# Kernel optimization log

Measured on AMD Instinct MI355X. Metric: run time of the kernel, lower is better.

The kernel has to match this reference:

```python
import jax, jax.numpy as jnp
import numpy as np

D = 2048
H = 32
EPS = 1e-5


def _ln(z, scale, bias):
    m = jnp.mean(z, axis=-1, keepdims=True)
    v = jnp.mean(jnp.square(z - m), axis=-1, keepdims=True)
    return (z - m) / jnp.sqrt(v + EPS) * scale + bias


def setup_inputs() -> dict:
    key = jax.random.key(0)
    ks = jax.random.split(key, 12)
    B, S = 4, 1024
    s = 0.02
    return {
        "x": jax.random.normal(ks[0], (B, S, D), jnp.float32),
        "Wq": jax.random.normal(ks[1], (D, D), jnp.float32) * s,
        "Wk": jax.random.normal(ks[2], (D, D), jnp.float32) * s,
        "Wv": jax.random.normal(ks[3], (D, D), jnp.float32) * s,
        "ln1_scale": jnp.ones((D,), jnp.float32) + jax.random.normal(ks[4], (D,), jnp.float32) * s,
        "ln1_bias": jax.random.normal(ks[5], (D,), jnp.float32) * s,
        "ln2_scale": jnp.ones((D,), jnp.float32) + jax.random.normal(ks[6], (D,), jnp.float32) * s,
        "ln2_bias": jax.random.normal(ks[7], (D,), jnp.float32) * s,
        "ff1_w": jax.random.normal(ks[8], (D, D), jnp.float32) * s,
        "ff1_b": jax.random.normal(ks[9], (D,), jnp.float32) * s,
        "ff2_w": jax.random.normal(ks[10], (D, D), jnp.float32) * s,
        "ff2_b": jax.random.normal(ks[11], (D,), jnp.float32) * s,
    }


def reference(x, Wq, Wk, Wv, ln1_scale, ln1_bias, ln2_scale, ln2_bias,
              ff1_w, ff1_b, ff2_w, ff2_b):
    B, S, _ = x.shape
    hd = D // H
    residual = x
    h = _ln(x, ln1_scale, ln1_bias)
    # QKV projections (no bias, per source)
    q = (h @ Wq).reshape(B, S, H, hd).transpose(0, 2, 1, 3)  # [B,H,S,hd]
    k = (h @ Wk).reshape(B, S, H, hd).transpose(0, 2, 1, 3)
    v = (h @ Wv).reshape(B, S, H, hd).transpose(0, 2, 1, 3)
    # NOTE: source scales by input_size**0.5 (full D), not head_dim
    scores = jnp.einsum('bhqd,bhkd->bhqk', q, k) / jnp.sqrt(jnp.float32(D))
    attn_probs = jax.nn.softmax(scores, axis=-1)  # [B,H,S,S]
    # attended_values is computed in the source but NEVER used (source bug, kept faithful)
    _attended = jnp.einsum('bhqk,bhkd->bhqd', attn_probs, v)
    del _attended
    x2 = h + residual  # source: x += residual, where x is LN1 output
    h2 = _ln(x2, ln2_scale, ln2_bias)
    ff = jnp.maximum(h2 @ ff1_w + ff1_b, 0.0) @ ff2_w + ff2_b
    out = ff + x2
    return out, attn_probs
```

## Files before the change

### kernel.cpp

```cpp
#include <hip/hip_runtime.h>
#include <math.h>


typedef unsigned short u16;
typedef u16    u16x8  __attribute__((ext_vector_type(8)));
typedef __bf16 bf16x8 __attribute__((ext_vector_type(8)));
typedef float  f32x4  __attribute__((ext_vector_type(4)));

#define MFMA16(a, b, c) __builtin_amdgcn_mfma_f32_16x16x32_bf16((a), (b), (c), 0, 0, 0)

__device__ __forceinline__ u16 f2bf(float f) {
  unsigned u = __builtin_bit_cast(unsigned, f);
  u += 0x7fffu + ((u >> 16) & 1u);
  return (u16)(u >> 16);
}

__device__ __forceinline__ void gload_lds16(const u16* g, u16* l) {
  __builtin_amdgcn_global_load_lds(
      (const __attribute__((address_space(1))) unsigned int*)g,
      (__attribute__((address_space(3))) unsigned int*)l, 16, 0, 0);
}

__global__ __launch_bounds__(256) void transpose_cast(const float* __restrict__ W,
                                                      u16* __restrict__ WT) {
  __shared__ u16 tile[64][65];
  const int n0 = blockIdx.x * 64, k0 = blockIdx.y * 64;
  const int c = threadIdx.x & 63, rb = threadIdx.x >> 6;
#pragma unroll
  for (int i = 0; i < 16; i++) {
    int r = rb + i * 4;
    tile[r][c] = f2bf(W[(size_t)(k0 + r) * 2048 + n0 + c]);
  }
  __syncthreads();
#pragma unroll
  for (int i = 0; i < 16; i++) {
    int r = rb + i * 4;
    WT[(size_t)(n0 + r) * 2048 + k0 + c] = tile[c][r];
  }
}

__device__ __forceinline__ float block_sum(float s, float* sbuf, int tid) {
#pragma unroll
  for (int off = 32; off; off >>= 1) s += __shfl_down(s, off, 64);
  __syncthreads();
  if ((tid & 63) == 0) sbuf[tid >> 6] = s;
  __syncthreads();
  return sbuf[0] + sbuf[1] + sbuf[2] + sbuf[3];
}

__global__ __launch_bounds__(256) void ln_fused(
    const float* __restrict__ x,
    const float* __restrict__ s1, const float* __restrict__ b1,
    const float* __restrict__ s2, const float* __restrict__ b2,
    u16* __restrict__ h_bf, float* __restrict__ x2o, u16* __restrict__ h2_bf) {
  __shared__ float sbuf[4];
  const int row = blockIdx.x, tid = threadIdx.x;
  const size_t rbase = (size_t)row * 2048;
  const int c = tid * 8;

  float v[8];
  *(float4*)&v[0] = *(const float4*)(x + rbase + c);
  *(float4*)&v[4] = *(const float4*)(x + rbase + c + 4);

  float s = 0.f;
#pragma unroll
  for (int i = 0; i < 8; i++) s += v[i];
  const float m1 = block_sum(s, sbuf, tid) * (1.f / 2048.f);
  float ss = 0.f;
#pragma unroll
  for (int i = 0; i < 8; i++) { float d = v[i] - m1; ss += d * d; }
  const float r1 = rsqrtf(block_sum(ss, sbuf, tid) * (1.f / 2048.f) + 1e-5f);

  float w[8], bb[8];
  *(float4*)&w[0] = *(const float4*)(s1 + c);
  *(float4*)&w[4] = *(const float4*)(s1 + c + 4);
  *(float4*)&bb[0] = *(const float4*)(b1 + c);
  *(float4*)&bb[4] = *(const float4*)(b1 + c + 4);

  float xx[8];
  u16x8 hv;
#pragma unroll
  for (int i = 0; i < 8; i++) {
    float hh = (v[i] - m1) * r1 * w[i] + bb[i];
    xx[i] = hh + v[i];
    hv[i] = f2bf(hh);
  }
  *(u16x8*)(h_bf + rbase + c) = hv;
  *(float4*)(x2o + rbase + c) = *(float4*)&xx[0];
  *(float4*)(x2o + rbase + c + 4) = *(float4*)&xx[4];

  s = 0.f;
#pragma unroll
  for (int i = 0; i < 8; i++) s += xx[i];
  const float m2 = block_sum(s, sbuf, tid) * (1.f / 2048.f);
  ss = 0.f;
#pragma unroll
  for (int i = 0; i < 8; i++) { float d = xx[i] - m2; ss += d * d; }
  const float r2 = rsqrtf(block_sum(ss, sbuf, tid) * (1.f / 2048.f) + 1e-5f);

  *(float4*)&w[0] = *(const float4*)(s2 + c);
  *(float4*)&w[4] = *(const float4*)(s2 + c + 4);
  *(float4*)&bb[0] = *(const float4*)(b2 + c);
  *(float4*)&bb[4] = *(const float4*)(b2 + c + 4);
#pragma unroll
  for (int i = 0; i < 8; i++) hv[i] = f2bf((xx[i] - m2) * r2 * w[i] + bb[i]);
  *(u16x8*)(h2_bf + rbase + c) = hv;
}

template <int BIAS, int RELU, int RESID, int OUTBF>
__global__ __launch_bounds__(256) void gemm_bf16(
    const u16* __restrict__ A, const u16* __restrict__ BT,
    const float* __restrict__ bias, const float* __restrict__ resid,
    void* __restrict__ Cout) {
  constexpr int K = 2048, N = 2048, BK = 64;
  __shared__ u16 As[128 * BK];
  __shared__ u16 Bs[128 * BK];
  const int tid = threadIdx.x;
  const int row0 = blockIdx.y * 128, col0 = blockIdx.x * 128;
  const int wid = tid >> 6, lane = tid & 63, lr = lane & 15, quad = lane >> 4;
  const int wr0 = (wid >> 1) * 64, wc0 = (wid & 1) * 64;
  const int srow = lane >> 3;
  const int scol = (lane & 7) * 8;

  f32x4 acc[4][4];
#pragma unroll
  for (int i = 0; i < 4; i++)
#pragma unroll
    for (int j = 0; j < 4; j++) acc[i][j] = (f32x4){0.f, 0.f, 0.f, 0.f};

  const u16* gA = A + (size_t)(row0 + srow) * K + scol;
  const u16* gB = BT + (size_t)(col0 + srow) * K + scol;

  for (int k0 = 0; k0 < K; k0 += BK) {
    if (k0) __syncthreads();
#pragma unroll
    for (int i = 0; i < 4; i++) {
      const int rg = i * 32 + wid * 8;
      gload_lds16(gA + (size_t)rg * K + k0, &As[rg * BK]);
      gload_lds16(gB + (size_t)rg * K + k0, &Bs[rg * BK]);
    }
    __syncthreads();

#pragma unroll
    for (int kk = 0; kk < 2; kk++) {
      bf16x8 af[4], bfr[4];
#pragma unroll
      for (int i = 0; i < 4; i++)
        af[i] = *(const bf16x8*)&As[(wr0 + i * 16 + lr) * BK + kk * 32 + quad * 8];
#pragma unroll
      for (int j = 0; j < 4; j++)
        bfr[j] = *(const bf16x8*)&Bs[(wc0 + j * 16 + lr) * BK + kk * 32 + quad * 8];
#pragma unroll
      for (int i = 0; i < 4; i++)
#pragma unroll
        for (int j = 0; j < 4; j++) acc[i][j] = MFMA16(af[i], bfr[j], acc[i][j]);
    }
  }

#pragma unroll
  for (int i = 0; i < 4; i++) {
#pragma unroll
    for (int r = 0; r < 4; r++) {
      const int row = row0 + wr0 + i * 16 + quad * 4 + r;
#pragma unroll
      for (int j = 0; j < 4; j++) {
        const int col = col0 + wc0 + j * 16 + lr;
        float v = acc[i][j][r];
        if (BIAS) v += bias[col];
        if (RELU) v = fmaxf(v, 0.f);
        if (RESID) v += resid[(size_t)row * N + col];
        if (OUTBF)
          ((u16*)Cout)[(size_t)row * N + col] = f2bf(v);
        else
          ((float*)Cout)[(size_t)row * N + col] = v;
      }
    }
  }
}

__global__ __launch_bounds__(256) void attn_kernel(const u16* __restrict__ qm,
                                                   const u16* __restrict__ km,
                                                   float* __restrict__ probs) {
  __shared__ float sc[16 * 1024];
  const int tid = threadIdx.x, wid = tid >> 6, lane = tid & 63;
  const int lr = lane & 15, quad = lane >> 4;
  const int q0 = blockIdx.x * 16, h = blockIdx.y, b = blockIdx.z;

  const size_t qbase = (size_t)(b * 1024 + q0 + lr) * 2048 + h * 64 + quad * 8;
  const bf16x8 a0 = *(const bf16x8*)(qm + qbase);
  const bf16x8 a1 = *(const bf16x8*)(qm + qbase + 32);
  const float scale = 0.022097086912079608f;

  for (int t = 0; t < 16; t++) {
    const int c0 = wid * 256 + t * 16;
    const size_t kbase = (size_t)(b * 1024 + c0 + lr) * 2048 + h * 64 + quad * 8;
    const bf16x8 b0 = *(const bf16x8*)(km + kbase);
    const bf16x8 b1 = *(const bf16x8*)(km + kbase + 32);
    f32x4 acc = (f32x4){0.f, 0.f, 0.f, 0.f};
    acc = MFMA16(a0, b0, acc);
    acc = MFMA16(a1, b1, acc);
#pragma unroll
    for (int r = 0; r < 4; r++) sc[(quad * 4 + r) * 1024 + c0 + lr] = acc[r] * scale;
  }
  __syncthreads();

#pragma unroll
  for (int rr = 0; rr < 4; rr++) {
    const int row = wid * 4 + rr;
    float vals[16];
    float mx = -1e30f;
#pragma unroll
    for (int i = 0; i < 16; i++) {
      vals[i] = sc[row * 1024 + lane + 64 * i];
      mx = fmaxf(mx, vals[i]);
    }
#pragma unroll
    for (int off = 32; off; off >>= 1) mx = fmaxf(mx, __shfl_xor(mx, off, 64));
    float sum = 0.f;
#pragma unroll
    for (int i = 0; i < 16; i++) {
      vals[i] = __expf(vals[i] - mx);
      sum += vals[i];
    }
#pragma unroll
    for (int off = 32; off; off >>= 1) sum += __shfl_xor(sum, off, 64);
    const float inv = 1.f / sum;
    float* pr = probs + (size_t)((b * 32 + h) * 1024 + q0 + row) * 1024;
#pragma unroll
    for (int i = 0; i < 16; i++) pr[lane + 64 * i] = vals[i] * inv;
  }
}

extern "C" void kernel_launch(void* const* d_in, const int* in_sizes, int n_in,
                              void* d_out, int out_size, void* d_ws, size_t ws_size,
                              hipStream_t stream) {
  const float* x = (const float*)d_in[0];
  const float* Wq = (const float*)d_in[1];
  const float* Wk = (const float*)d_in[2];
  const float* ln1s = (const float*)d_in[4];
  const float* ln1b = (const float*)d_in[5];
  const float* ln2s = (const float*)d_in[6];
  const float* ln2b = (const float*)d_in[7];
  const float* f1w = (const float*)d_in[8];
  const float* f1b = (const float*)d_in[9];
  const float* f2w = (const float*)d_in[10];
  const float* f2b = (const float*)d_in[11];

  char* p = (char*)d_ws;
  const size_t WSZ = (size_t)2048 * 2048 * 2;
  const size_t ASZ = (size_t)4096 * 2048 * 2;
  u16* WqT = (u16*)p; p += WSZ;
  u16* WkT = (u16*)p; p += WSZ;
  u16* F1T = (u16*)p; p += WSZ;
  u16* F2T = (u16*)p; p += WSZ;
  u16* h_bf = (u16*)p; p += ASZ;
  u16* h2_bf = (u16*)p; p += ASZ;
  u16* q_bf = (u16*)p; p += ASZ;
  u16* k_bf = (u16*)p; p += ASZ;
  u16* a1_bf = (u16*)p; p += ASZ;
  float* x2 = (float*)p; p += (size_t)4096 * 2048 * 4;

  float* out = (float*)d_out;
  float* probs = out + (size_t)4096 * 2048;

  const dim3 tg(32, 32);
  transpose_cast<<<tg, 256, 0, stream>>>(Wq, WqT);
  transpose_cast<<<tg, 256, 0, stream>>>(Wk, WkT);
  transpose_cast<<<tg, 256, 0, stream>>>(f1w, F1T);
  transpose_cast<<<tg, 256, 0, stream>>>(f2w, F2T);

  ln_fused<<<4096, 256, 0, stream>>>(x, ln1s, ln1b, ln2s, ln2b, h_bf, x2, h2_bf);

  const dim3 gg(16, 32);
  gemm_bf16<0, 0, 0, 1><<<gg, 256, 0, stream>>>(h_bf, WqT, nullptr, nullptr, q_bf);
  gemm_bf16<0, 0, 0, 1><<<gg, 256, 0, stream>>>(h_bf, WkT, nullptr, nullptr, k_bf);

  attn_kernel<<<dim3(64, 32, 4), 256, 0, stream>>>(q_bf, k_bf, probs);

  gemm_bf16<1, 1, 0, 1><<<gg, 256, 0, stream>>>(h2_bf, F1T, f1b, nullptr, a1_bf);
  gemm_bf16<1, 0, 1, 0><<<gg, 256, 0, stream>>>(a1_bf, F2T, f2b, x2, out);
}
```

Measured before the change: 1.006 ms.

## Fuse Q/K GEMMs and weight transposes, warp-per-row LN, vectorize softmax IO

```diff
diff --git a/kernel.cpp b/kernel.cpp
--- a/kernel.cpp
+++ b/kernel.cpp
@@ -3,6 +3,7 @@
 
 
 typedef unsigned short u16;
+typedef u16    u16x4  __attribute__((ext_vector_type(4)));
 typedef u16    u16x8  __attribute__((ext_vector_type(8)));
 typedef __bf16 bf16x8 __attribute__((ext_vector_type(8)));
 typedef float  f32x4  __attribute__((ext_vector_type(4)));
@@ -21,9 +22,14 @@
       (__attribute__((address_space(3))) unsigned int*)l, 16, 0, 0);
 }
 
-__global__ __launch_bounds__(256) void transpose_cast(const float* __restrict__ W,
-                                                      u16* __restrict__ WT) {
+__global__ __launch_bounds__(256) void transpose_cast4(
+    const float* __restrict__ W0, const float* __restrict__ W1,
+    const float* __restrict__ W2, const float* __restrict__ W3,
+    u16* __restrict__ dst) {
   __shared__ u16 tile[64][65];
+  const int z = blockIdx.z;
+  const float* W = (z == 0) ? W0 : (z == 1) ? W1 : (z == 2) ? W2 : W3;
+  u16* WT = dst + (size_t)z * 2048 * 2048;
   const int n0 = blockIdx.x * 64, k0 = blockIdx.y * 64;
   const int c = threadIdx.x & 63, rb = threadIdx.x >> 6;
 #pragma unroll
@@ -37,15 +43,6 @@
     int r = rb + i * 4;
     WT[(size_t)(n0 + r) * 2048 + k0 + c] = tile[c][r];
   }
-}
-
-__device__ __forceinline__ float block_sum(float s, float* sbuf, int tid) {
-#pragma unroll
-  for (int off = 32; off; off >>= 1) s += __shfl_down(s, off, 64);
-  __syncthreads();
-  if ((tid & 63) == 0) sbuf[tid >> 6] = s;
-  __syncthreads();
-  return sbuf[0] + sbuf[1] + sbuf[2] + sbuf[3];
 }
 
 __global__ __launch_bounds__(256) void ln_fused(
@@ -53,66 +50,78 @@
     const float* __restrict__ s1, const float* __restrict__ b1,
     const float* __restrict__ s2, const float* __restrict__ b2,
     u16* __restrict__ h_bf, float* __restrict__ x2o, u16* __restrict__ h2_bf) {
-  __shared__ float sbuf[4];
-  const int row = blockIdx.x, tid = threadIdx.x;
-  const size_t rbase = (size_t)row * 2048;
-  const int c = tid * 8;
-
-  float v[8];
-  *(float4*)&v[0] = *(const float4*)(x + rbase + c);
-  *(float4*)&v[4] = *(const float4*)(x + rbase + c + 4);
+  const int wid = threadIdx.x >> 6, lane = threadIdx.x & 63;
+  const size_t rbase = (size_t)(blockIdx.x * 4 + wid) * 2048;
+
+  float v[32];
+#pragma unroll
+  for (int i = 0; i < 8; i++)
+    *(float4*)&v[i * 4] = *(const float4*)(x + rbase + i * 256 + lane * 4);
 
   float s = 0.f;
 #pragma unroll
-  for (int i = 0; i < 8; i++) s += v[i];
-  const float m1 = block_sum(s, sbuf, tid) * (1.f / 2048.f);
+  for (int i = 0; i < 32; i++) s += v[i];
+#pragma unroll
+  for (int off = 32; off; off >>= 1) s += __shfl_xor(s, off, 64);
+  const float m1 = s * (1.f / 2048.f);
+
   float ss = 0.f;
 #pragma unroll
-  for (int i = 0; i < 8; i++) { float d = v[i] - m1; ss += d * d; }
-  const float r1 = rsqrtf(block_sum(ss, sbuf, tid) * (1.f / 2048.f) + 1e-5f);
-
-  float w[8], bb[8];
-  *(float4*)&w[0] = *(const float4*)(s1 + c);
-  *(float4*)&w[4] = *(const float4*)(s1 + c + 4);
-  *(float4*)&bb[0] = *(const float4*)(b1 + c);
-  *(float4*)&bb[4] = *(const float4*)(b1 + c + 4);
-
-  float xx[8];
-  u16x8 hv;
+  for (int i = 0; i < 32; i++) { float d = v[i] - m1; ss += d * d; }
+#pragma unroll
+  for (int off = 32; off; off >>= 1) ss += __shfl_xor(ss, off, 64);
+  const float r1 = rsqrtf(ss * (1.f / 2048.f) + 1e-5f);
+
+  float xx[32];
 #pragma unroll
   for (int i = 0; i < 8; i++) {
-    float hh = (v[i] - m1) * r1 * w[i] + bb[i];
-    xx[i] = hh + v[i];
-    hv[i] = f2bf(hh);
-  }
-  *(u16x8*)(h_bf + rbase + c) = hv;
-  *(float4*)(x2o + rbase + c) = *(float4*)&xx[0];
-  *(float4*)(x2o + rbase + c + 4) = *(float4*)&xx[4];
+    const int c = i * 256 + lane * 4;
+    float4 w4 = *(const float4*)(s1 + c);
+    float4 b4 = *(const float4*)(b1 + c);
+    u16x4 hv;
+#pragma unroll
+    for (int j = 0; j < 4; j++) {
+      float hh = (v[i * 4 + j] - m1) * r1 * (&w4.x)[j] + (&b4.x)[j];
+      xx[i * 4 + j] = hh + v[i * 4 + j];
+      hv[j] = f2bf(hh);
+    }
+    *(u16x4*)(h_bf + rbase + c) = hv;
+    *(float4*)(x2o + rbase + c) = *(float4*)&xx[i * 4];
+  }
 
   s = 0.f;
 #pragma unroll
-  for (int i = 0; i < 8; i++) s += xx[i];
-  const float m2 = block_sum(s, sbuf, tid) * (1.f / 2048.f);
+  for (int i = 0; i < 32; i++) s += xx[i];
+#pragma unroll
+  for (int off = 32; off; off >>= 1) s += __shfl_xor(s, off, 64);
+  const float m2 = s * (1.f / 2048.f);
+
   ss = 0.f;
 #pragma unroll
-  for (int i = 0; i < 8; i++) { float d = xx[i] - m2; ss += d * d; }
-  const float r2 = rsqrtf(block_sum(ss, sbuf, tid) * (1.f / 2048.f) + 1e-5f);
-
-  *(float4*)&w[0] = *(const float4*)(s2 + c);
-  *(float4*)&w[4] = *(const float4*)(s2 + c + 4);
-  *(float4*)&bb[0] = *(const float4*)(b2 + c);
-  *(float4*)&bb[4] = *(const float4*)(b2 + c + 4);
-#pragma unroll
-  for (int i = 0; i < 8; i++) hv[i] = f2bf((xx[i] - m2) * r2 * w[i] + bb[i]);
-  *(u16x8*)(h2_bf + rbase + c) = hv;
-}
-
-template <int BIAS, int RELU, int RESID, int OUTBF>
+  for (int i = 0; i < 32; i++) { float d = xx[i] - m2; ss += d * d; }
+#pragma unroll
+  for (int off = 32; off; off >>= 1) ss += __shfl_xor(ss, off, 64);
+  const float r2 = rsqrtf(ss * (1.f / 2048.f) + 1e-5f);
+
+#pragma unroll
+  for (int i = 0; i < 8; i++) {
+    const int c = i * 256 + lane * 4;
+    float4 w4 = *(const float4*)(s2 + c);
+    float4 b4 = *(const float4*)(b2 + c);
+    u16x4 hv;
+#pragma unroll
+    for (int j = 0; j < 4; j++)
+      hv[j] = f2bf((xx[i * 4 + j] - m2) * r2 * (&w4.x)[j] + (&b4.x)[j]);
+    *(u16x4*)(h2_bf + rbase + c) = hv;
+  }
+}
+
+template <int N, int BIAS, int RELU, int RESID, int OUTBF>
 __global__ __launch_bounds__(256) void gemm_bf16(
     const u16* __restrict__ A, const u16* __restrict__ BT,
     const float* __restrict__ bias, const float* __restrict__ resid,
     void* __restrict__ Cout) {
-  constexpr int K = 2048, N = 2048, BK = 64;
+  constexpr int K = 2048, BK = 64;
   __shared__ u16 As[128 * BK];
   __shared__ u16 Bs[128 * BK];
   const int tid = threadIdx.x;
@@ -178,24 +187,23 @@
   }
 }
 
-__global__ __launch_bounds__(256) void attn_kernel(const u16* __restrict__ qm,
-                                                   const u16* __restrict__ km,
+__global__ __launch_bounds__(256) void attn_kernel(const u16* __restrict__ qk,
                                                    float* __restrict__ probs) {
   __shared__ float sc[16 * 1024];
   const int tid = threadIdx.x, wid = tid >> 6, lane = tid & 63;
   const int lr = lane & 15, quad = lane >> 4;
   const int q0 = blockIdx.x * 16, h = blockIdx.y, b = blockIdx.z;
 
-  const size_t qbase = (size_t)(b * 1024 + q0 + lr) * 2048 + h * 64 + quad * 8;
-  const bf16x8 a0 = *(const bf16x8*)(qm + qbase);
-  const bf16x8 a1 = *(const bf16x8*)(qm + qbase + 32);
+  const size_t qbase = (size_t)(b * 1024 + q0 + lr) * 4096 + h * 64 + quad * 8;
+  const bf16x8 a0 = *(const bf16x8*)(qk + qbase);
+  const bf16x8 a1 = *(const bf16x8*)(qk + qbase + 32);
   const float scale = 0.022097086912079608f;
 
   for (int t = 0; t < 16; t++) {
     const int c0 = wid * 256 + t * 16;
-    const size_t kbase = (size_t)(b * 1024 + c0 + lr) * 2048 + h * 64 + quad * 8;
-    const bf16x8 b0 = *(const bf16x8*)(km + kbase);
-    const bf16x8 b1 = *(const bf16x8*)(km + kbase + 32);
+    const size_t kbase = (size_t)(b * 1024 + c0 + lr) * 4096 + 2048 + h * 64 + quad * 8;
+    const bf16x8 b0 = *(const bf16x8*)(qk + kbase);
+    const bf16x8 b1 = *(const bf16x8*)(qk + kbase + 32);
     f32x4 acc = (f32x4){0.f, 0.f, 0.f, 0.f};
     acc = MFMA16(a0, b0, acc);
     acc = MFMA16(a1, b1, acc);
@@ -208,12 +216,12 @@
   for (int rr = 0; rr < 4; rr++) {
     const int row = wid * 4 + rr;
     float vals[16];
+#pragma unroll
+    for (int i = 0; i < 4; i++)
+      *(float4*)&vals[i * 4] = *(const float4*)&sc[row * 1024 + i * 256 + lane * 4];
     float mx = -1e30f;
 #pragma unroll
-    for (int i = 0; i < 16; i++) {
-      vals[i] = sc[row * 1024 + lane + 64 * i];
-      mx = fmaxf(mx, vals[i]);
-    }
+    for (int i = 0; i < 16; i++) mx = fmaxf(mx, vals[i]);
 #pragma unroll
     for (int off = 32; off; off >>= 1) mx = fmaxf(mx, __shfl_xor(mx, off, 64));
     float sum = 0.f;
@@ -227,7 +235,12 @@
     const float inv = 1.f / sum;
     float* pr = probs + (size_t)((b * 32 + h) * 1024 + q0 + row) * 1024;
 #pragma unroll
-    for (int i = 0; i < 16; i++) pr[lane + 64 * i] = vals[i] * inv;
+    for (int i = 0; i < 4; i++) {
+      float4 o;
+#pragma unroll
+      for (int j = 0; j < 4; j++) (&o.x)[j] = vals[i * 4 + j] * inv;
+      *(float4*)&pr[i * 256 + lane * 4] = o;
+    }
   }
 }
 
@@ -249,34 +262,28 @@
   char* p = (char*)d_ws;
   const size_t WSZ = (size_t)2048 * 2048 * 2;
   const size_t ASZ = (size_t)4096 * 2048 * 2;
-  u16* WqT = (u16*)p; p += WSZ;
-  u16* WkT = (u16*)p; p += WSZ;
+  u16* WqkT = (u16*)p; p += 2 * WSZ;
   u16* F1T = (u16*)p; p += WSZ;
   u16* F2T = (u16*)p; p += WSZ;
   u16* h_bf = (u16*)p; p += ASZ;
   u16* h2_bf = (u16*)p; p += ASZ;
-  u16* q_bf = (u16*)p; p += ASZ;
-  u16* k_bf = (u16*)p; p += ASZ;
+  u16* qk_bf = (u16*)p; p += 2 * ASZ;
   u16* a1_bf = (u16*)p; p += ASZ;
   float* x2 = (float*)p; p += (size_t)4096 * 2048 * 4;
 
   float* out = (float*)d_out;
   float* probs = out + (size_t)4096 * 2048;
 
-  const dim3 tg(32, 32);
-  transpose_cast<<<tg, 256, 0, stream>>>(Wq, WqT);
-  transpose_cast<<<tg, 256, 0, stream>>>(Wk, WkT);
-  transpose_cast<<<tg, 256, 0, stream>>>(f1w, F1T);
-  transpose_cast<<<tg, 256, 0, stream>>>(f2w, F2T);
-
-  ln_fused<<<4096, 256, 0, stream>>>(x, ln1s, ln1b, ln2s, ln2b, h_bf, x2, h2_bf);
+  transpose_cast4<<<dim3(32, 32, 4), 256, 0, stream>>>(Wq, Wk, f1w, f2w, WqkT);
+
+  ln_fused<<<1024, 256, 0, stream>>>(x, ln1s, ln1b, ln2s, ln2b, h_bf, x2, h2_bf);
+
+  gemm_bf16<4096, 0, 0, 0, 1><<<dim3(32, 32), 256, 0, stream>>>(
+      h_bf, WqkT, nullptr, nullptr, qk_bf);
+
+  attn_kernel<<<dim3(64, 32, 4), 256, 0, stream>>>(qk_bf, probs);
 
   const dim3 gg(16, 32);
-  gemm_bf16<0, 0, 0, 1><<<gg, 256, 0, stream>>>(h_bf, WqT, nullptr, nullptr, q_bf);
-  gemm_bf16<0, 0, 0, 1><<<gg, 256, 0, stream>>>(h_bf, WkT, nullptr, nullptr, k_bf);
-
-  attn_kernel<<<dim3(64, 32, 4), 256, 0, stream>>>(q_bf, k_bf, probs);
-
-  gemm_bf16<1, 1, 0, 1><<<gg, 256, 0, stream>>>(h2_bf, F1T, f1b, nullptr, a1_bf);
-  gemm_bf16<1, 0, 1, 0><<<gg, 256, 0, stream>>>(a1_bf, F2T, f2b, x2, out);
-}
+  gemm_bf16<2048, 1, 1, 0, 1><<<gg, 256, 0, stream>>>(h2_bf, F1T, f1b, nullptr, a1_bf);
+  gemm_bf16<2048, 1, 0, 1, 0><<<gg, 256, 0, stream>>>(a1_bf, F2T, f2b, x2, out);
+}
```

New measurement: 985.5 us. -2.1%, faster.
